# Performance work log

Measured on AMD Instinct MI355X. Metric: run time of the kernel, lower is better.

## Reference

```python
import jax, jax.numpy as jnp
import numpy as np

B, C, H, W = 4, 256, 48, 48
HEADS, DIM_HEAD, SCALE = 8, 64, 10.0
INNER = HEADS * DIM_HEAD
EPS = 1e-12


def setup_inputs() -> dict:
    key = jax.random.key(0)
    k1, k2, k3, k4 = jax.random.split(key, 4)
    x = jax.random.normal(k1, (B, C, H, W), dtype=jnp.float32)
    # 1x1 conv weights stored as [out_ch, in_ch]
    w_qkv = jax.random.normal(k2, (3 * INNER, C), dtype=jnp.float32) * (1.0 / np.sqrt(C))
    w_out = jax.random.normal(k3, (C, INNER), dtype=jnp.float32) * (1.0 / np.sqrt(INNER))
    b_out = jax.random.normal(k4, (C,), dtype=jnp.float32) * 0.01
    return {"x": x, "w_qkv": w_qkv, "w_out": w_out, "b_out": b_out}


def _l2norm(t):
    # normalize along last axis, clamping the norm at EPS (matches torch l2norm)
    denom = jnp.maximum(jnp.linalg.norm(t, axis=-1, keepdims=True), EPS)
    return t / denom


def reference(x, w_qkv, w_out, b_out):
    b, c, h, w = x.shape
    n = h * w
    # 1x1 conv QKV projection: [B, 3*INNER, H, W]
    qkv = jnp.einsum('oc,bchw->bohw', w_qkv, x)
    q, k, v = jnp.split(qkv, 3, axis=1)
    # [B, heads, dim_head, N] -> [B, heads, N, dim_head]
    def to_bhnd(t):
        return t.reshape(b, HEADS, DIM_HEAD, n).transpose(0, 1, 3, 2)
    q = _l2norm(to_bhnd(q))
    k = _l2norm(to_bhnd(k))
    v = to_bhnd(v)
    sim = jnp.einsum('bhid,bhjd->bhij', q, k) * SCALE  # [B,h,N,N]
    attn = jax.nn.softmax(sim, axis=-1)
    out = jnp.einsum('bhij,bhjd->bhid', attn, v)  # [B,h,N,d]
    # back to [B, INNER, H, W]
    out = out.transpose(0, 1, 3, 2).reshape(b, INNER, h, w)
    # 1x1 conv output projection with bias
    out = jnp.einsum('oc,bchw->bohw', w_out, out) + b_out[None, :, None, None]
    return out
```

## Files before the change

### kernel.cpp

```cpp
#include <hip/hip_runtime.h>

typedef unsigned short u16;
typedef __attribute__((ext_vector_type(8))) short bf16x8;
typedef __attribute__((ext_vector_type(4))) float f32x4;

#define MFMA16(A,B,C) __builtin_amdgcn_mfma_f32_16x16x32_bf16(A,B,C,0,0,0)

#define B_ 4
#define C_ 256
#define N_ 2304
#define HEADS_ 8
#define DH_ 64
#define INNER_ 512
#define SCALE_LOG2E 14.426950408889634f

__device__ __forceinline__ u16 f2bf(float f) {
    union { float f; unsigned int u; } v; v.f = f;
    unsigned int r = v.u + 0x7fffu + ((v.u >> 16) & 1u);
    return (u16)(r >> 16);
}
__device__ __forceinline__ float bf2f(u16 h) {
    union { unsigned int u; float f; } v; v.u = ((unsigned int)h) << 16;
    return v.f;
}
__device__ __forceinline__ unsigned int cvtpk(float a, float b) {
    unsigned int r;
    asm("v_cvt_pk_bf16_f32 %0, %1, %2" : "=v"(r) : "v"(a), "v"(b));
    return r;
}

__global__ __launch_bounds__(256) void k_prep(const float* __restrict__ x,
                                              u16* __restrict__ xT,
                                              const float* __restrict__ w_qkv,
                                              u16* __restrict__ wqb,
                                              const float* __restrict__ w_out,
                                              u16* __restrict__ wob) {
    __shared__ float tile[64][65];
    int idx = blockIdx.x;
    int t = threadIdx.x;
    if (idx < 576) {
        int b = idx / 144, rem = idx % 144;
        int n0 = (rem >> 2) * 64, c0 = (rem & 3) * 64;
        const float* xb = x + (size_t)b * C_ * N_;
        u16* xTb = xT + (size_t)b * N_ * C_;
        int r = t >> 4;
        int q4 = (t & 15) * 4;
#pragma unroll
        for (int pass = 0; pass < 4; ++pass) {
            int c = r + pass * 16;
            float4 v = *(const float4*)(xb + (size_t)(c0 + c) * N_ + n0 + q4);
            tile[c][q4+0] = v.x; tile[c][q4+1] = v.y; tile[c][q4+2] = v.z; tile[c][q4+3] = v.w;
        }
        __syncthreads();
#pragma unroll
        for (int pass = 0; pass < 4; ++pass) {
            int n = r + pass * 16;
            ushort4 o;
            o.x = f2bf(tile[q4+0][n]); o.y = f2bf(tile[q4+1][n]);
            o.z = f2bf(tile[q4+2][n]); o.w = f2bf(tile[q4+3][n]);
            *(ushort4*)(xTb + (size_t)(n0 + n) * C_ + c0 + q4) = o;
        }
    } else if (idx < 960) {
        int i = (idx - 576) * 256 + t;
        float4 v = ((const float4*)w_qkv)[i];
        ushort4 o;
        o.x = f2bf(v.x); o.y = f2bf(v.y); o.z = f2bf(v.z); o.w = f2bf(v.w);
        ((ushort4*)wqb)[i] = o;
    } else {
        int i = (idx - 960) * 256 + t;
        float4 v = ((const float4*)w_out)[i];
        ushort4 o;
        o.x = f2bf(v.x); o.y = f2bf(v.y); o.z = f2bf(v.z); o.w = f2bf(v.w);
        ((ushort4*)wob)[i] = o;
    }
}

__global__ __launch_bounds__(256) void k_qkv(const u16* __restrict__ w_qkv,
                                             const u16* __restrict__ xT,
                                             u16* __restrict__ Qn,
                                             u16* __restrict__ Kn,
                                             u16* __restrict__ Vt) {
    __shared__ __align__(16) u16 Wt[64][264];
    __shared__ __align__(16) u16 Xt[64][264];
    int mt = blockIdx.x, nt = blockIdx.y, b = blockIdx.z;
    int tid = threadIdx.x;
    int wv = tid >> 6, lane = tid & 63;
    int col = lane & 15, quad = lane >> 4;
    int o0 = mt * 64;
    const u16* wtile = w_qkv + (size_t)o0 * C_;
    const u16* xtile = xT + ((size_t)b * N_ + nt*64) * C_;
#pragma unroll
    for (int p = 0; p < 8; ++p) {
        int c = p * 256 + tid;
        int row = c >> 5, seg = c & 31;
        *(uint4*)(&Wt[row][seg*8]) = *(const uint4*)(wtile + (size_t)row * C_ + seg*8);
        *(uint4*)(&Xt[row][seg*8]) = *(const uint4*)(xtile + (size_t)row * C_ + seg*8);
    }
    __syncthreads();
    f32x4 z = {0.f, 0.f, 0.f, 0.f};
    f32x4 acc[4]; acc[0]=z; acc[1]=z; acc[2]=z; acc[3]=z;
#pragma unroll
    for (int ks = 0; ks < 8; ++ks) {
        bf16x8 bfrag = *(const bf16x8*)(&Xt[wv*16 + col][ks*32 + quad*8]);
#pragma unroll
        for (int mb = 0; mb < 4; ++mb) {
            bf16x8 afrag = *(const bf16x8*)(&Wt[mb*16 + col][ks*32 + quad*8]);
            acc[mb] = MFMA16(afrag, bfrag, acc[mb]);
        }
    }
    int n = nt * 64 + wv * 16 + col;
    int which = mt >> 3, h = mt & 7;
    if (which < 2) {
        float s = 0.f;
#pragma unroll
        for (int mb = 0; mb < 4; ++mb)
#pragma unroll
            for (int r = 0; r < 4; ++r) s += acc[mb][r] * acc[mb][r];
        s += __shfl_xor(s, 16);
        s += __shfl_xor(s, 32);
        float inv = 1.f / fmaxf(sqrtf(s), 1e-12f);
        if (which == 0) inv *= SCALE_LOG2E;
        u16* dst = (which == 0 ? Qn : Kn) + (((size_t)b * HEADS_ + h) * N_ + n) * DH_;
#pragma unroll
        for (int mb = 0; mb < 4; ++mb) {
            uint2 o;
            o.x = cvtpk(acc[mb][0] * inv, acc[mb][1] * inv);
            o.y = cvtpk(acc[mb][2] * inv, acc[mb][3] * inv);
            *(uint2*)(dst + mb*16 + quad*4) = o;
        }
    } else {
        u16* dst = Vt + ((size_t)b * HEADS_ + h) * (size_t)DH_ * N_;
#pragma unroll
        for (int mb = 0; mb < 4; ++mb)
#pragma unroll
            for (int r = 0; r < 4; ++r)
                dst[(size_t)(mb*16 + quad*4 + r) * N_ + n] = f2bf(acc[mb][r]);
    }
}

__global__ __launch_bounds__(256) void k_attn_split(const u16* __restrict__ Qn,
                                                    const u16* __restrict__ Kn,
                                                    const u16* __restrict__ Vt,
                                                    u16* __restrict__ Opb,
                                                    float* __restrict__ lp) {
    __shared__ __align__(16) u16 Kt[64][72];
    __shared__ __align__(16) u16 Vtl[64][72];
    __shared__ __align__(16) u16 plds[4][32][72];
    int head_lin = blockIdx.x & 31;
    int rest = blockIdx.x >> 5;
    int qt = rest % 18;
    int ksplit = rest / 18;
    int b = head_lin >> 3, h = head_lin & 7;
    int tid = threadIdx.x;
    int wv = tid >> 6, lane = tid & 63;
    int col = lane & 15, quad = lane >> 4;
    size_t head = (size_t)b * HEADS_ + h;
    const u16* Qh = Qn + head * (size_t)N_ * DH_;
    const u16* Kh = Kn + head * (size_t)N_ * DH_ + (size_t)ksplit * 576 * DH_;
    const u16* Vh = Vt + head * (size_t)DH_ * N_;
    int q0 = qt * 128 + wv * 32;
    bf16x8 qfA0 = *(const bf16x8*)(Qh + (size_t)(q0 + col) * DH_ + quad*8);
    bf16x8 qfA1 = *(const bf16x8*)(Qh + (size_t)(q0 + col) * DH_ + 32 + quad*8);
    bf16x8 qfB0 = *(const bf16x8*)(Qh + (size_t)(q0 + 16 + col) * DH_ + quad*8);
    bf16x8 qfB1 = *(const bf16x8*)(Qh + (size_t)(q0 + 16 + col) * DH_ + 32 + quad*8);
    f32x4 z = {0.f, 0.f, 0.f, 0.f};
    f32x4 OA[4], OB[4];
#pragma unroll
    for (int i = 0; i < 4; ++i) { OA[i] = z; OB[i] = z; }
    float lA = 0.f, lB = 0.f;
    int srow = tid >> 3, sseg = tid & 7;
    const u16* ksrc0 = Kh + (size_t)tid * 8;
    const u16* vsrc0 = Vh + (size_t)srow * N_ + ksplit * 576 + sseg * 8;

    uint4 k0 = *(const uint4*)(ksrc0);
    uint4 k1 = *(const uint4*)(ksrc0 + 2048);
    uint4 v0 = *(const uint4*)(vsrc0);
    uint4 v1 = *(const uint4*)(vsrc0 + (size_t)32 * N_);

    for (int kt = 0; kt < 9; ++kt) {
        *(uint4*)(&Kt[srow][sseg*8])      = k0;
        *(uint4*)(&Kt[32 + srow][sseg*8]) = k1;
        *(uint4*)(&Vtl[srow][sseg*8])      = v0;
        *(uint4*)(&Vtl[32 + srow][sseg*8]) = v1;
        __syncthreads();
        int ktn = kt + 1 < 9 ? kt + 1 : kt;
        k0 = *(const uint4*)(ksrc0 + (size_t)ktn * 4096);
        k1 = *(const uint4*)(ksrc0 + (size_t)ktn * 4096 + 2048);
        v0 = *(const uint4*)(vsrc0 + ktn * 64);
        v1 = *(const uint4*)(vsrc0 + (size_t)32 * N_ + ktn * 64);
        float rsA = 0.f, rsB = 0.f;
#pragma unroll
        for (int nb = 0; nb < 4; ++nb) {
            bf16x8 kf0 = *(const bf16x8*)(&Kt[nb*16 + col][quad*8]);
            bf16x8 kf1 = *(const bf16x8*)(&Kt[nb*16 + col][32 + quad*8]);
            f32x4 a = MFMA16(kf0, qfA0, z);
            a = MFMA16(kf1, qfA1, a);
            f32x4 c = MFMA16(kf0, qfB0, z);
            c = MFMA16(kf1, qfB1, c);
            float a0 = exp2f(a[0]);
            float a1 = exp2f(a[1]);
            float a2 = exp2f(a[2]);
            float a3 = exp2f(a[3]);
            float c0 = exp2f(c[0]);
            float c1 = exp2f(c[1]);
            float c2 = exp2f(c[2]);
            float c3 = exp2f(c[3]);
            rsA += (a0 + a1) + (a2 + a3);
            rsB += (c0 + c1) + (c2 + c3);
            uint2 wA, wB;
            wA.x = cvtpk(a0, a1); wA.y = cvtpk(a2, a3);
            wB.x = cvtpk(c0, c1); wB.y = cvtpk(c2, c3);
            *(uint2*)(&plds[wv][col][nb*16 + quad*4]) = wA;
            *(uint2*)(&plds[wv][16 + col][nb*16 + quad*4]) = wB;
        }
        lA += rsA; lB += rsB;
        __asm__ volatile("" ::: "memory");
#pragma unroll
        for (int ks = 0; ks < 2; ++ks) {
            bf16x8 pfA = *(const bf16x8*)(&plds[wv][col][ks*32 + quad*8]);
            bf16x8 pfB = *(const bf16x8*)(&plds[wv][16 + col][ks*32 + quad*8]);
#pragma unroll
            for (int nb = 0; nb < 4; ++nb) {
                bf16x8 vf = *(const bf16x8*)(&Vtl[nb*16 + col][ks*32 + quad*8]);
                OA[nb] = MFMA16(vf, pfA, OA[nb]);
                OB[nb] = MFMA16(vf, pfB, OB[nb]);
            }
        }
        __asm__ volatile("" ::: "memory");
        __syncthreads();
    }
    lA += __shfl_xor(lA, 16); lA += __shfl_xor(lA, 32);
    lB += __shfl_xor(lB, 16); lB += __shfl_xor(lB, 32);
    u16* dstA = Opb + (((size_t)ksplit * B_ + b) * N_ + q0 + col) * INNER_ + h * DH_;
    u16* dstB = dstA + (size_t)16 * INNER_;
#pragma unroll
    for (int nb = 0; nb < 4; ++nb) {
        uint2 wA, wB;
        wA.x = cvtpk(OA[nb][0], OA[nb][1]); wA.y = cvtpk(OA[nb][2], OA[nb][3]);
        wB.x = cvtpk(OB[nb][0], OB[nb][1]); wB.y = cvtpk(OB[nb][2], OB[nb][3]);
        *(uint2*)(dstA + nb*16 + quad*4) = wA;
        *(uint2*)(dstB + nb*16 + quad*4) = wB;
    }
    if (quad == 0) {
        size_t lbase = (((size_t)ksplit * B_ + b) * HEADS_ + h) * N_;
        lp[lbase + q0 + col] = lA;
        lp[lbase + q0 + 16 + col] = lB;
    }
}

__global__ __launch_bounds__(256) void k_comb(const u16* __restrict__ Opb,
                                              const float* __restrict__ lp,
                                              u16* __restrict__ AO) {
    int g = blockIdx.x * 256 + threadIdx.x;
    int b = g / 294912;
    int rem = g % 294912;
    int n = rem >> 7;
    int i4 = rem & 127;
    int h = i4 >> 4;
    float s0 = 0.f, s1 = 0.f, s2 = 0.f, s3 = 0.f, l = 0.f;
#pragma unroll
    for (int s = 0; s < 4; ++s) {
        ushort4 p = ((const ushort4*)Opb)[g + (size_t)s * 1179648];
        s0 += bf2f(p.x); s1 += bf2f(p.y); s2 += bf2f(p.z); s3 += bf2f(p.w);
        l += lp[(((size_t)s * B_ + b) * HEADS_ + h) * N_ + n];
    }
    float inv = 1.f / l;
    uint2 o;
    o.x = cvtpk(s0 * inv, s1 * inv);
    o.y = cvtpk(s2 * inv, s3 * inv);
    ((uint2*)AO)[g] = o;
}

__global__ __launch_bounds__(256) void k_attn(const u16* __restrict__ Qn,
                                              const u16* __restrict__ Kn,
                                              const u16* __restrict__ Vt,
                                              u16* __restrict__ AO) {
    __shared__ __align__(16) u16 Kt[64][72];
    __shared__ __align__(16) u16 Vtl[64][72];
    __shared__ __align__(16) u16 plds[4][32][72];
    int head_lin = blockIdx.x & 31;
    int qt = blockIdx.x >> 5;
    int b = head_lin >> 3, h = head_lin & 7;
    int tid = threadIdx.x;
    int wv = tid >> 6, lane = tid & 63;
    int col = lane & 15, quad = lane >> 4;
    size_t head = (size_t)b * HEADS_ + h;
    const u16* Qh = Qn + head * (size_t)N_ * DH_;
    const u16* Kh = Kn + head * (size_t)N_ * DH_;
    const u16* Vh = Vt + head * (size_t)DH_ * N_;
    int q0 = qt * 128 + wv * 32;
    bf16x8 qfA0 = *(const bf16x8*)(Qh + (size_t)(q0 + col) * DH_ + quad*8);
    bf16x8 qfA1 = *(const bf16x8*)(Qh + (size_t)(q0 + col) * DH_ + 32 + quad*8);
    bf16x8 qfB0 = *(const bf16x8*)(Qh + (size_t)(q0 + 16 + col) * DH_ + quad*8);
    bf16x8 qfB1 = *(const bf16x8*)(Qh + (size_t)(q0 + 16 + col) * DH_ + 32 + quad*8);
    f32x4 z = {0.f, 0.f, 0.f, 0.f};
    f32x4 OA[4], OB[4];
#pragma unroll
    for (int i = 0; i < 4; ++i) { OA[i] = z; OB[i] = z; }
    float lA = 0.f, lB = 0.f;
    int srow = tid >> 3, sseg = tid & 7;
    const u16* ksrc0 = Kh + (size_t)tid * 8;
    const u16* vsrc0 = Vh + (size_t)srow * N_ + sseg * 8;
    uint4 k0 = *(const uint4*)(ksrc0);
    uint4 k1 = *(const uint4*)(ksrc0 + 2048);
    uint4 v0 = *(const uint4*)(vsrc0);
    uint4 v1 = *(const uint4*)(vsrc0 + (size_t)32 * N_);
    for (int kt = 0; kt < N_/64; ++kt) {
        *(uint4*)(&Kt[srow][sseg*8])      = k0;
        *(uint4*)(&Kt[32 + srow][sseg*8]) = k1;
        *(uint4*)(&Vtl[srow][sseg*8])      = v0;
        *(uint4*)(&Vtl[32 + srow][sseg*8]) = v1;
        __syncthreads();
        int ktn = kt + 1 < N_/64 ? kt + 1 : kt;
        k0 = *(const uint4*)(ksrc0 + (size_t)ktn * 4096);
        k1 = *(const uint4*)(ksrc0 + (size_t)ktn * 4096 + 2048);
        v0 = *(const uint4*)(vsrc0 + ktn * 64);
        v1 = *(const uint4*)(vsrc0 + (size_t)32 * N_ + ktn * 64);
        float rsA = 0.f, rsB = 0.f;
#pragma unroll
        for (int nb = 0; nb < 4; ++nb) {
            bf16x8 kf0 = *(const bf16x8*)(&Kt[nb*16 + col][quad*8]);
            bf16x8 kf1 = *(const bf16x8*)(&Kt[nb*16 + col][32 + quad*8]);
            f32x4 a = MFMA16(kf0, qfA0, z);
            a = MFMA16(kf1, qfA1, a);
            f32x4 c = MFMA16(kf0, qfB0, z);
            c = MFMA16(kf1, qfB1, c);
            float a0 = exp2f(a[0]);
            float a1 = exp2f(a[1]);
            float a2 = exp2f(a[2]);
            float a3 = exp2f(a[3]);
            float c0 = exp2f(c[0]);
            float c1 = exp2f(c[1]);
            float c2 = exp2f(c[2]);
            float c3 = exp2f(c[3]);
            rsA += (a0 + a1) + (a2 + a3);
            rsB += (c0 + c1) + (c2 + c3);
            uint2 wA, wB;
            wA.x = cvtpk(a0, a1); wA.y = cvtpk(a2, a3);
            wB.x = cvtpk(c0, c1); wB.y = cvtpk(c2, c3);
            *(uint2*)(&plds[wv][col][nb*16 + quad*4]) = wA;
            *(uint2*)(&plds[wv][16 + col][nb*16 + quad*4]) = wB;
        }
        lA += rsA; lB += rsB;
        __asm__ volatile("" ::: "memory");
#pragma unroll
        for (int ks = 0; ks < 2; ++ks) {
            bf16x8 pfA = *(const bf16x8*)(&plds[wv][col][ks*32 + quad*8]);
            bf16x8 pfB = *(const bf16x8*)(&plds[wv][16 + col][ks*32 + quad*8]);
#pragma unroll
            for (int nb = 0; nb < 4; ++nb) {
                bf16x8 vf = *(const bf16x8*)(&Vtl[nb*16 + col][ks*32 + quad*8]);
                OA[nb] = MFMA16(vf, pfA, OA[nb]);
                OB[nb] = MFMA16(vf, pfB, OB[nb]);
            }
        }
        __asm__ volatile("" ::: "memory");
        __syncthreads();
    }
    lA += __shfl_xor(lA, 16); lA += __shfl_xor(lA, 32);
    lB += __shfl_xor(lB, 16); lB += __shfl_xor(lB, 32);
    float linvA = 1.f / lA, linvB = 1.f / lB;
    u16* dstA = AO + ((size_t)b * N_ + q0 + col) * INNER_ + h * DH_;
    u16* dstB = AO + ((size_t)b * N_ + q0 + 16 + col) * INNER_ + h * DH_;
#pragma unroll
    for (int nb = 0; nb < 4; ++nb) {
        uint2 wA, wB;
        wA.x = cvtpk(OA[nb][0] * linvA, OA[nb][1] * linvA);
        wA.y = cvtpk(OA[nb][2] * linvA, OA[nb][3] * linvA);
        wB.x = cvtpk(OB[nb][0] * linvB, OB[nb][1] * linvB);
        wB.y = cvtpk(OB[nb][2] * linvB, OB[nb][3] * linvB);
        *(uint2*)(dstA + nb*16 + quad*4) = wA;
        *(uint2*)(dstB + nb*16 + quad*4) = wB;
    }
}

__global__ __launch_bounds__(256) void k_proj(const u16* __restrict__ w_out,
                                              const float* __restrict__ b_out,
                                              const u16* __restrict__ AO,
                                              float* __restrict__ out) {
    __shared__ __align__(16) u16 Wt[64][264];
    __shared__ __align__(16) u16 At[64][264];
    int mt = blockIdx.x, nt = blockIdx.y, b = blockIdx.z;
    int tid = threadIdx.x;
    int wv = tid >> 6, lane = tid & 63;
    int col = lane & 15, quad = lane >> 4;
    int o0b = mt * 64;
    const u16* wtile = w_out + (size_t)o0b * INNER_;
    const u16* atile = AO + ((size_t)b * N_ + nt*64) * INNER_;
    f32x4 z = {0.f, 0.f, 0.f, 0.f};
    f32x4 acc[4]; acc[0]=z; acc[1]=z; acc[2]=z; acc[3]=z;
#pragma unroll
    for (int half = 0; half < 2; ++half) {
        if (half) __syncthreads();
#pragma unroll
        for (int p = 0; p < 8; ++p) {
            int c = p * 256 + tid;
            int row = c >> 5, seg = c & 31;
            *(uint4*)(&Wt[row][seg*8]) =
                *(const uint4*)(wtile + (size_t)row * INNER_ + half*256 + seg*8);
            *(uint4*)(&At[row][seg*8]) =
                *(const uint4*)(atile + (size_t)row * INNER_ + half*256 + seg*8);
        }
        __syncthreads();
#pragma unroll
        for (int ks = 0; ks < 8; ++ks) {
            bf16x8 af = *(const bf16x8*)(&Wt[wv*16 + col][ks*32 + quad*8]);
#pragma unroll
            for (int nb = 0; nb < 4; ++nb) {
                bf16x8 bfv = *(const bf16x8*)(&At[nb*16 + col][ks*32 + quad*8]);
                acc[nb] = MFMA16(af, bfv, acc[nb]);
            }
        }
    }
    int o0 = o0b + wv * 16;
    float bias[4];
#pragma unroll
    for (int r = 0; r < 4; ++r) bias[r] = b_out[o0 + quad*4 + r];
    float* dst = out + ((size_t)b * C_ + o0) * N_ + nt*64;
#pragma unroll
    for (int nb = 0; nb < 4; ++nb)
#pragma unroll
        for (int r = 0; r < 4; ++r)
            dst[(size_t)(quad*4 + r) * N_ + nb*16 + col] = acc[nb][r] + bias[r];
}

extern "C" void kernel_launch(void* const* d_in, const int* in_sizes, int n_in,
                              void* d_out, int out_size, void* d_ws, size_t ws_size,
                              hipStream_t stream) {
    const float* x     = (const float*)d_in[0];
    const float* w_qkv = (const float*)d_in[1];
    const float* w_out = (const float*)d_in[2];
    const float* b_out = (const float*)d_in[3];
    float* out = (float*)d_out;

    char* ws = (char*)d_ws;
    u16* xT  = (u16*)(ws);
    u16* Qn  = (u16*)(ws + 4718592);
    u16* Kn  = (u16*)(ws + 14155776);
    u16* Vt  = (u16*)(ws + 23592960);
    u16* AO  = (u16*)(ws + 33030144);
    u16* wqb = (u16*)(ws + 42467328);
    u16* wob = (u16*)(ws + 43253760);
    u16* Opb = (u16*)(ws + 43515904);
    float* lp = (float*)(ws + 1179648);
    const size_t need = 81854464;

    hipLaunchKernelGGL(k_prep, dim3(1088), dim3(256), 0, stream, x, xT, w_qkv, wqb, w_out, wob);
    hipLaunchKernelGGL(k_qkv,  dim3(24, N_/64, B_), dim3(256), 0, stream, wqb, xT, Qn, Kn, Vt);
    if (ws_size >= need) {
        hipLaunchKernelGGL(k_attn_split, dim3(2304), dim3(256), 0, stream, Qn, Kn, Vt, Opb, lp);
        hipLaunchKernelGGL(k_comb, dim3(4608), dim3(256), 0, stream, Opb, lp, AO);
    } else {
        hipLaunchKernelGGL(k_attn, dim3((N_/128) * 32), dim3(256), 0, stream, Qn, Kn, Vt, AO);
    }
    hipLaunchKernelGGL(k_proj, dim3(C_/64, N_/64, B_), dim3(256), 0, stream, wob, b_out, AO, out);
}
```

Measured before the change: 184.2 us.

## Switch attention kernel to 32x32x16 MFMA with register-resident P via permlane32 swap

Rewrites the split-K attention inner loop to use 32x32x16 bf16 MFMA tiles instead of 16x16x32. The softmax probabilities are kept in registers and rearranged into the B-operand layout with v_permlane32_swap, so the per-wave LDS staging buffer for P and its write/read round trip are removed. Larger MFMA tiles mean fewer LDS fragment reads per FLOP, but accumulator register pressure rises and correctness depends on the permlane lane mapping matching the MFMA layouts.

```diff
diff --git a/kernel.cpp b/kernel.cpp
--- a/kernel.cpp
+++ b/kernel.cpp
@@ -3,8 +3,10 @@
 typedef unsigned short u16;
 typedef __attribute__((ext_vector_type(8))) short bf16x8;
 typedef __attribute__((ext_vector_type(4))) float f32x4;
+typedef __attribute__((ext_vector_type(16))) float f32x16;
 
 #define MFMA16(A,B,C) __builtin_amdgcn_mfma_f32_16x16x32_bf16(A,B,C,0,0,0)
+#define MFMA32(A,B,C) __builtin_amdgcn_mfma_f32_32x32x16_bf16(A,B,C,0,0,0)
 
 #define B_ 4
 #define C_ 256
@@ -27,6 +29,9 @@
     unsigned int r;
     asm("v_cvt_pk_bf16_f32 %0, %1, %2" : "=v"(r) : "v"(a), "v"(b));
     return r;
+}
+__device__ __forceinline__ void pl32swap(unsigned &a, unsigned &b) {
+    asm volatile("v_permlane32_swap_b32 %0, %1" : "+v"(a), "+v"(b));
 }
 
 __global__ __launch_bounds__(256) void k_prep(const float* __restrict__ x,
@@ -138,6 +143,19 @@
     }
 }
 
+__device__ __forceinline__ void store_o32(const f32x16 O, u16* dst, int hi) {
+    unsigned c0 = cvtpk(O[0], O[1]),  c1 = cvtpk(O[2], O[3]);
+    unsigned c2 = cvtpk(O[4], O[5]),  c3 = cvtpk(O[6], O[7]);
+    unsigned c4 = cvtpk(O[8], O[9]),  c5 = cvtpk(O[10], O[11]);
+    unsigned c6 = cvtpk(O[12], O[13]), c7 = cvtpk(O[14], O[15]);
+    pl32swap(c0, c2); pl32swap(c1, c3);
+    pl32swap(c4, c6); pl32swap(c5, c7);
+    uint4 w0; w0.x = c0; w0.y = c1; w0.z = c2; w0.w = c3;
+    uint4 w1; w1.x = c4; w1.y = c5; w1.z = c6; w1.w = c7;
+    *(uint4*)(dst + hi*8)      = w0;
+    *(uint4*)(dst + 16 + hi*8) = w1;
+}
+
 __global__ __launch_bounds__(256) void k_attn_split(const u16* __restrict__ Qn,
                                                     const u16* __restrict__ Kn,
                                                     const u16* __restrict__ Vt,
@@ -145,7 +163,6 @@
                                                     float* __restrict__ lp) {
     __shared__ __align__(16) u16 Kt[64][72];
     __shared__ __align__(16) u16 Vtl[64][72];
-    __shared__ __align__(16) u16 plds[4][32][72];
     int head_lin = blockIdx.x & 31;
     int rest = blockIdx.x >> 5;
     int qt = rest % 18;
@@ -153,21 +170,20 @@
     int b = head_lin >> 3, h = head_lin & 7;
     int tid = threadIdx.x;
     int wv = tid >> 6, lane = tid & 63;
-    int col = lane & 15, quad = lane >> 4;
+    int q32 = lane & 31, hi = lane >> 5;
     size_t head = (size_t)b * HEADS_ + h;
     const u16* Qh = Qn + head * (size_t)N_ * DH_;
     const u16* Kh = Kn + head * (size_t)N_ * DH_ + (size_t)ksplit * 576 * DH_;
     const u16* Vh = Vt + head * (size_t)DH_ * N_;
     int q0 = qt * 128 + wv * 32;
-    bf16x8 qfA0 = *(const bf16x8*)(Qh + (size_t)(q0 + col) * DH_ + quad*8);
-    bf16x8 qfA1 = *(const bf16x8*)(Qh + (size_t)(q0 + col) * DH_ + 32 + quad*8);
-    bf16x8 qfB0 = *(const bf16x8*)(Qh + (size_t)(q0 + 16 + col) * DH_ + quad*8);
-    bf16x8 qfB1 = *(const bf16x8*)(Qh + (size_t)(q0 + 16 + col) * DH_ + 32 + quad*8);
-    f32x4 z = {0.f, 0.f, 0.f, 0.f};
-    f32x4 OA[4], OB[4];
-#pragma unroll
-    for (int i = 0; i < 4; ++i) { OA[i] = z; OB[i] = z; }
-    float lA = 0.f, lB = 0.f;
+    bf16x8 qf[4];
+#pragma unroll
+    for (int ds = 0; ds < 4; ++ds)
+        qf[ds] = *(const bf16x8*)(Qh + (size_t)(q0 + q32) * DH_ + ds*16 + hi*8);
+    f32x16 accO0, accO1;
+#pragma unroll
+    for (int i = 0; i < 16; ++i) { accO0[i] = 0.f; accO1[i] = 0.f; }
+    float lsum = 0.f;
     int srow = tid >> 3, sseg = tid & 7;
     const u16* ksrc0 = Kh + (size_t)tid * 8;
     const u16* vsrc0 = Vh + (size_t)srow * N_ + ksplit * 576 + sseg * 8;
@@ -188,63 +204,47 @@
         k1 = *(const uint4*)(ksrc0 + (size_t)ktn * 4096 + 2048);
         v0 = *(const uint4*)(vsrc0 + ktn * 64);
         v1 = *(const uint4*)(vsrc0 + (size_t)32 * N_ + ktn * 64);
-        float rsA = 0.f, rsB = 0.f;
-#pragma unroll
-        for (int nb = 0; nb < 4; ++nb) {
-            bf16x8 kf0 = *(const bf16x8*)(&Kt[nb*16 + col][quad*8]);
-            bf16x8 kf1 = *(const bf16x8*)(&Kt[nb*16 + col][32 + quad*8]);
-            f32x4 a = MFMA16(kf0, qfA0, z);
-            a = MFMA16(kf1, qfA1, a);
-            f32x4 c = MFMA16(kf0, qfB0, z);
-            c = MFMA16(kf1, qfB1, c);
-            float a0 = exp2f(a[0]);
-            float a1 = exp2f(a[1]);
-            float a2 = exp2f(a[2]);
-            float a3 = exp2f(a[3]);
-            float c0 = exp2f(c[0]);
-            float c1 = exp2f(c[1]);
-            float c2 = exp2f(c[2]);
-            float c3 = exp2f(c[3]);
-            rsA += (a0 + a1) + (a2 + a3);
-            rsB += (c0 + c1) + (c2 + c3);
-            uint2 wA, wB;
-            wA.x = cvtpk(a0, a1); wA.y = cvtpk(a2, a3);
-            wB.x = cvtpk(c0, c1); wB.y = cvtpk(c2, c3);
-            *(uint2*)(&plds[wv][col][nb*16 + quad*4]) = wA;
-            *(uint2*)(&plds[wv][16 + col][nb*16 + quad*4]) = wB;
-        }
-        lA += rsA; lB += rsB;
-        __asm__ volatile("" ::: "memory");
-#pragma unroll
-        for (int ks = 0; ks < 2; ++ks) {
-            bf16x8 pfA = *(const bf16x8*)(&plds[wv][col][ks*32 + quad*8]);
-            bf16x8 pfB = *(const bf16x8*)(&plds[wv][16 + col][ks*32 + quad*8]);
-#pragma unroll
-            for (int nb = 0; nb < 4; ++nb) {
-                bf16x8 vf = *(const bf16x8*)(&Vtl[nb*16 + col][ks*32 + quad*8]);
-                OA[nb] = MFMA16(vf, pfA, OA[nb]);
-                OB[nb] = MFMA16(vf, pfB, OB[nb]);
+#pragma unroll
+        for (int kb = 0; kb < 2; ++kb) {
+            f32x16 s;
+#pragma unroll
+            for (int i = 0; i < 16; ++i) s[i] = 0.f;
+#pragma unroll
+            for (int ds = 0; ds < 4; ++ds) {
+                bf16x8 kf = *(const bf16x8*)(&Kt[kb*32 + q32][ds*16 + hi*8]);
+                s = MFMA32(kf, qf[ds], s);
             }
-        }
-        __asm__ volatile("" ::: "memory");
-        __syncthreads();
-    }
-    lA += __shfl_xor(lA, 16); lA += __shfl_xor(lA, 32);
-    lB += __shfl_xor(lB, 16); lB += __shfl_xor(lB, 32);
-    u16* dstA = Opb + (((size_t)ksplit * B_ + b) * N_ + q0 + col) * INNER_ + h * DH_;
-    u16* dstB = dstA + (size_t)16 * INNER_;
-#pragma unroll
-    for (int nb = 0; nb < 4; ++nb) {
-        uint2 wA, wB;
-        wA.x = cvtpk(OA[nb][0], OA[nb][1]); wA.y = cvtpk(OA[nb][2], OA[nb][3]);
-        wB.x = cvtpk(OB[nb][0], OB[nb][1]); wB.y = cvtpk(OB[nb][2], OB[nb][3]);
-        *(uint2*)(dstA + nb*16 + quad*4) = wA;
-        *(uint2*)(dstB + nb*16 + quad*4) = wB;
-    }
-    if (quad == 0) {
+#pragma unroll
+            for (int i = 0; i < 16; ++i) s[i] = exp2f(s[i]);
+            lsum += ( ((s[0]+s[1])+(s[2]+s[3])) + ((s[4]+s[5])+(s[6]+s[7])) )
+                  + ( ((s[8]+s[9])+(s[10]+s[11])) + ((s[12]+s[13])+(s[14]+s[15])) );
+            unsigned c0 = cvtpk(s[0], s[1]),  c1 = cvtpk(s[2], s[3]);
+            unsigned c2 = cvtpk(s[4], s[5]),  c3 = cvtpk(s[6], s[7]);
+            unsigned c4 = cvtpk(s[8], s[9]),  c5 = cvtpk(s[10], s[11]);
+            unsigned c6 = cvtpk(s[12], s[13]), c7 = cvtpk(s[14], s[15]);
+            pl32swap(c0, c2); pl32swap(c1, c3);
+            pl32swap(c4, c6); pl32swap(c5, c7);
+            union { unsigned u[4]; bf16x8 v; } pf0, pf1;
+            pf0.u[0] = c0; pf0.u[1] = c1; pf0.u[2] = c2; pf0.u[3] = c3;
+            pf1.u[0] = c4; pf1.u[1] = c5; pf1.u[2] = c6; pf1.u[3] = c7;
+            bf16x8 vf00 = *(const bf16x8*)(&Vtl[q32][kb*32 + hi*8]);
+            bf16x8 vf01 = *(const bf16x8*)(&Vtl[32 + q32][kb*32 + hi*8]);
+            accO0 = MFMA32(vf00, pf0.v, accO0);
+            accO1 = MFMA32(vf01, pf0.v, accO1);
+            bf16x8 vf10 = *(const bf16x8*)(&Vtl[q32][kb*32 + 16 + hi*8]);
+            bf16x8 vf11 = *(const bf16x8*)(&Vtl[32 + q32][kb*32 + 16 + hi*8]);
+            accO0 = MFMA32(vf10, pf1.v, accO0);
+            accO1 = MFMA32(vf11, pf1.v, accO1);
+        }
+        __syncthreads();
+    }
+    lsum += __shfl_xor(lsum, 32);
+    u16* dst = Opb + (((size_t)ksplit * B_ + b) * N_ + q0 + q32) * INNER_ + h * DH_;
+    store_o32(accO0, dst, hi);
+    store_o32(accO1, dst + 32, hi);
+    if (hi == 0) {
         size_t lbase = (((size_t)ksplit * B_ + b) * HEADS_ + h) * N_;
-        lp[lbase + q0 + col] = lA;
-        lp[lbase + q0 + 16 + col] = lB;
+        lp[lbase + q0 + q32] = lsum;
     }
 }
 
```

Result: no change. 183.4 us (-0.5%).
